# Kernel tuning notes

Measured on AMD Instinct MI355X. Metric: run time of the kernel, lower is better.

Reference implementation:

```python
import jax, jax.numpy as jnp
import numpy as np
from jax import lax

NUM_DISP = 64
BLOCK = 21
EPS = 1e-12  # F.normalize default eps


def _box_sum(v):
    # v: (N, H, W) -> BLOCK x BLOCK zero-padded box sum (same shape), separable.
    p = BLOCK // 2
    v = v[:, None]  # (N,1,H,W)
    kv = jnp.ones((1, 1, BLOCK, 1), v.dtype)
    kh = jnp.ones((1, 1, 1, BLOCK), v.dtype)
    v = lax.conv_general_dilated(v, kv, (1, 1), ((p, p), (0, 0)))
    v = lax.conv_general_dilated(v, kh, (1, 1), ((0, 0), (p, p)))
    return v[:, 0]


def _l2norm_c(img):
    n = jnp.sqrt(jnp.sum(img * img, axis=1, keepdims=True))
    return img / jnp.maximum(n, EPS)


def _disparity(left, right):
    # left, right: (B, 3, H, W)
    left = _l2norm_c(left)
    right = _l2norm_c(right)
    B, C, H, W = left.shape
    d = jnp.arange(NUM_DISP)
    xs = jnp.arange(W)
    idx = xs[None, :] - d[:, None]              # (D, W): source column in right image
    valid = (idx >= 0)
    r_shift = right[:, :, :, jnp.clip(idx, 0)]  # (B, C, H, D, W)
    r_shift = jnp.where(valid[None, None, None], r_shift, 0.0)
    # per-pixel channel-summed absolute difference -> (B, D, H, W)
    diff = jnp.sum(jnp.abs(left[:, :, :, None, :] - r_shift), axis=1)  # (B, H, D, W)
    diff = jnp.transpose(diff, (0, 2, 1, 3))    # (B, D, H, W)
    cost = _box_sum(diff.reshape(B * NUM_DISP, H, W)).reshape(B, NUM_DISP, H, W)
    cost = cost / (C * BLOCK * BLOCK)           # mean SAD over block elements
    return jnp.argmin(cost, axis=1).astype(left.dtype)  # (B, H, W)


def setup_inputs() -> dict:
    key = jax.random.key(0)
    k1, k2 = jax.random.split(key)
    x = jax.random.normal(k1, (2, 6, 320, 512), dtype=jnp.float32)
    gt = jax.random.normal(k2, (2, 6, 320, 512), dtype=jnp.float32)
    return {"x": x, "gt": gt}


def reference(x, gt):
    disp_gt = _disparity(gt[:, :3], gt[:, 3:])
    disp_pred = _disparity(x[:, :3], x[:, 3:])
    return jnp.mean(jnp.abs(disp_pred - disp_gt))
```

## Files before the change

### kernel.cpp

```cpp
#include <hip/hip_runtime.h>
#include <math.h>

constexpr int B = 2, H = 320, W = 512, D = 64;
constexpr int HW = H * W;
constexpr int R = 10;
constexpr int SEG = 80;
constexpr int NSEG = H / SEG;
constexpr int RS = 548;
constexpr float EPS = 1e-12f;

__global__ void k_norm(const float* __restrict__ x, const float* __restrict__ gt,
                       float4* __restrict__ nrm4) {
    int idx = blockIdx.x * blockDim.x + threadIdx.x;
    if (idx >= 2 * B * HW) return;
    int t = idx / (B * HW);
    int rem = idx - t * (B * HW);
    int b = rem / HW;
    int hw = rem - b * HW;
    const float* p = (t == 0 ? x : gt) + (size_t)b * 6 * HW + hw;
    float v0 = p[0],      v1 = p[HW],     v2 = p[2 * HW];
    float v3 = p[3 * HW], v4 = p[4 * HW], v5 = p[5 * HW];
    float n1 = fmaxf(sqrtf(v0 * v0 + v1 * v1 + v2 * v2), EPS);
    float n2 = fmaxf(sqrtf(v3 * v3 + v4 * v4 + v5 * v5), EPS);
    float4* q = nrm4 + (size_t)(t * B + b) * 2 * HW + hw;
    q[0]  = make_float4(v0 / n1, v1 / n1, v2 / n1, 0.f);
    q[HW] = make_float4(v3 / n2, v4 / n2, v5 / n2, 0.f);
}

__global__ __launch_bounds__(512, 2) void k_cost(const float4* __restrict__ nrm4,
                                                 float* __restrict__ cost, int t) {
    int blk = blockIdx.x;
    int combo = blk & 7;
    int d = blk >> 3;
    int b = combo >> 2;
    int seg = combo & 3;
    int w = threadIdx.x;
    const float4* L4 = nrm4 + (size_t)(t * B + b) * 2 * HW;
    const float4* R4 = L4 + HW;
    const bool val = (w >= d);
    const int wr = val ? (w - d) : 0;
    const int h0 = seg * SEG;

    __shared__ float ring[21][W];
    __shared__ float vsb[2][8][RS];

    {
        int j = w >> 6, k = w & 63;
        if (k < 10)      { vsb[0][j][k] = 0.f;       vsb[1][j][k] = 0.f; }
        else if (k < 20) { vsb[0][j][512 + k] = 0.f; vsb[1][j][512 + k] = 0.f; }
    }

    auto diff = [&](int h) -> float {
        float4 l = L4[(size_t)h * W + w];
        if (val) {
            float4 r = R4[(size_t)h * W + wr];
            return fabsf(l.x - r.x) + fabsf(l.y - r.y) + fabsf(l.z - r.z);
        }
        return fabsf(l.x) + fabsf(l.y) + fabsf(l.z);
    };

    float vs = 0.f;
    for (int k = 0; k < 20; ++k) {
        int h = h0 - R + k;
        float dv0 = (h >= 0) ? diff(h) : 0.f;
        ring[k][w] = dv0;
        vs += dv0;
    }
    ring[20][w] = 0.f;

    float* cp = cost + ((size_t)(b * D + d) * H) * W;
    const int cc = threadIdx.x >> 3;
    const int jj = threadIdx.x & 7;

    int slot0 = 20;
    for (int ss = 0; ss < SEG / 8; ++ss) {
        int sl[8];
        float dold[8], dv[8];
#pragma unroll
        for (int j = 0; j < 8; ++j) { int s2 = slot0 + j; if (s2 >= 21) s2 -= 21; sl[j] = s2; }
#pragma unroll
        for (int j = 0; j < 8; ++j) dold[j] = ring[sl[j]][w];
#pragma unroll
        for (int j = 0; j < 8; ++j) {
            int hn = h0 + ss * 8 + j + R;
            dv[j] = (hn < H) ? diff(hn) : 0.f;
        }
#pragma unroll
        for (int j = 0; j < 8; ++j) ring[sl[j]][w] = dv[j];
        float* vrow = &vsb[ss & 1][0][0];
#pragma unroll
        for (int j = 0; j < 8; ++j) { vs += dv[j] - dold[j]; vrow[j * RS + 10 + w] = vs; }
        __syncthreads();
        const float* vp = &vsb[ss & 1][jj][8 * cc];
        float wnd[28];
#pragma unroll
        for (int q = 0; q < 7; ++q) {
            float4 v4 = *(const float4*)(vp + 4 * q);
            wnd[4 * q] = v4.x; wnd[4 * q + 1] = v4.y;
            wnd[4 * q + 2] = v4.z; wnd[4 * q + 3] = v4.w;
        }
        float o = 0.f;
#pragma unroll
        for (int k = 0; k < 21; ++k) o += wnd[k];
        float out[8];
        out[0] = o;
#pragma unroll
        for (int k = 1; k < 8; ++k) { o += wnd[20 + k] - wnd[k - 1]; out[k] = o; }
        float* op = cp + (size_t)(h0 + ss * 8 + jj) * W + 8 * cc;
        *(float4*)(op)     = make_float4(out[0], out[1], out[2], out[3]);
        *(float4*)(op + 4) = make_float4(out[4], out[5], out[6], out[7]);
        slot0 += 8; if (slot0 >= 21) slot0 -= 21;
    }
}

__global__ void k_argmin0(const float* __restrict__ cost, float* __restrict__ disp) {
    int idx = blockIdx.x * 256 + threadIdx.x;
    if (idx >= B * HW) return;
    int b = idx / HW, hw = idx - b * HW;
    const float* cp = cost + (size_t)b * D * HW + hw;
    float best = cp[0]; int bd = 0;
#pragma unroll 16
    for (int d = 1; d < D; ++d) {
        float v = cp[(size_t)d * HW];
        if (v < best) { best = v; bd = d; }
    }
    disp[idx] = (float)bd;
}

__global__ void k_argmin1(const float* __restrict__ cost, const float* __restrict__ disp0,
                          float* __restrict__ part) {
    int idx = blockIdx.x * 256 + threadIdx.x;
    float s = 0.f;
    if (idx < B * HW) {
        int b = idx / HW, hw = idx - b * HW;
        const float* cp = cost + (size_t)b * D * HW + hw;
        float best = cp[0]; int bd = 0;
#pragma unroll 16
        for (int d = 1; d < D; ++d) {
            float v = cp[(size_t)d * HW];
            if (v < best) { best = v; bd = d; }
        }
        s = fabsf((float)bd - disp0[idx]);
    }
    __shared__ float sm[256];
    sm[threadIdx.x] = s;
    __syncthreads();
    for (int off = 128; off; off >>= 1) {
        if (threadIdx.x < off) sm[threadIdx.x] += sm[threadIdx.x + off];
        __syncthreads();
    }
    if (!threadIdx.x) part[blockIdx.x] = sm[0];
}

__global__ void k_red2(const float* __restrict__ part, float* __restrict__ out,
                       int nb, float inv) {
    __shared__ float sm[256];
    int tid = threadIdx.x;
    float s = 0.f;
    for (int i = tid; i < nb; i += 256) s += part[i];
    sm[tid] = s;
    __syncthreads();
    for (int off = 128; off; off >>= 1) {
        if (tid < off) sm[tid] += sm[tid + off];
        __syncthreads();
    }
    if (!tid) out[0] = sm[0] * inv;
}

extern "C" void kernel_launch(void* const* d_in, const int* in_sizes, int n_in,
                              void* d_out, int out_size, void* d_ws, size_t ws_size,
                              hipStream_t stream) {
    const float* x  = (const float*)d_in[0];
    const float* gt = (const float*)d_in[1];

    float4* nrm4 = (float4*)d_ws;
    float* cost  = (float*)(nrm4 + (size_t)2 * B * 2 * HW);
    float* disp  = cost + (size_t)B * D * HW;
    float* part  = disp + (size_t)2 * B * HW;

    constexpr int NPIX_BLKS = (B * HW + 255) / 256;

    k_norm<<<(2 * B * HW + 255) / 256, 256, 0, stream>>>(x, gt, nrm4);

    k_cost<<<B * NSEG * D, 512, 0, stream>>>(nrm4, cost, 0);
    k_argmin0<<<NPIX_BLKS, 256, 0, stream>>>(cost, disp);
    k_cost<<<B * NSEG * D, 512, 0, stream>>>(nrm4, cost, 1);
    k_argmin1<<<NPIX_BLKS, 256, 0, stream>>>(cost, disp, part);

    k_red2<<<1, 256, 0, stream>>>(part, (float*)d_out, NPIX_BLKS, 1.f / (float)(B * HW));
}
```

Measured before the change: 205.1 us.

## Fuse first argmin into second cost kernel and move ring buffer to registers

The argmin over the first image pair's cost volume now runs inside the second cost kernel. Each block reads a slice of the previous cost volume interleaved with its own work, which removes a separate argmin launch and lets those reads overlap with compute. This needs a second cost buffer in the workspace, with a fallback path when the workspace is too small. The 21-row shared-memory ring buffer becomes a fully unrolled 24-entry register ring, and the diff is made branch-free. This frees LDS but raises register pressure under launch bounds of 512 threads and 2 blocks.

Measured after the change: 198.4 us. 3.3% less time.

```diff
diff --git a/kernel.cpp b/kernel.cpp
--- a/kernel.cpp
+++ b/kernel.cpp
@@ -27,23 +27,24 @@
     q[HW] = make_float4(v3 / n2, v4 / n2, v5 / n2, 0.f);
 }
 
+template<bool FUSE>
 __global__ __launch_bounds__(512, 2) void k_cost(const float4* __restrict__ nrm4,
-                                                 float* __restrict__ cost, int t) {
-    int blk = blockIdx.x;
-    int combo = blk & 7;
-    int d = blk >> 3;
-    int b = combo >> 2;
-    int seg = combo & 3;
-    int w = threadIdx.x;
+                                                 float* __restrict__ cost,
+                                                 const float* __restrict__ cprev,
+                                                 float* __restrict__ dprev, int t) {
+    const int blk = blockIdx.x;
+    const int combo = blk & 7;
+    const int d = blk >> 3;
+    const int b = combo >> 2;
+    const int seg = combo & 3;
+    const int w = threadIdx.x;
     const float4* L4 = nrm4 + (size_t)(t * B + b) * 2 * HW;
     const float4* R4 = L4 + HW;
     const bool val = (w >= d);
     const int wr = val ? (w - d) : 0;
     const int h0 = seg * SEG;
 
-    __shared__ float ring[21][W];
     __shared__ float vsb[2][8][RS];
-
     {
         int j = w >> 6, k = w & 63;
         if (k < 10)      { vsb[0][j][k] = 0.f;       vsb[1][j][k] = 0.f; }
@@ -52,44 +53,71 @@
 
     auto diff = [&](int h) -> float {
         float4 l = L4[(size_t)h * W + w];
-        if (val) {
-            float4 r = R4[(size_t)h * W + wr];
-            return fabsf(l.x - r.x) + fabsf(l.y - r.y) + fabsf(l.z - r.z);
-        }
-        return fabsf(l.x) + fabsf(l.y) + fabsf(l.z);
+        float4 r = R4[(size_t)h * W + wr];
+        float a = fabsf(l.x - r.x) + fabsf(l.y - r.y) + fabsf(l.z - r.z);
+        float s = fabsf(l.x) + fabsf(l.y) + fabsf(l.z);
+        return val ? a : s;
     };
 
+    float ring[24];
     float vs = 0.f;
+#pragma unroll
     for (int k = 0; k < 20; ++k) {
         int h = h0 - R + k;
-        float dv0 = (h >= 0) ? diff(h) : 0.f;
-        ring[k][w] = dv0;
-        vs += dv0;
-    }
-    ring[20][w] = 0.f;
-
-    float* cp = cost + ((size_t)(b * D + d) * H) * W;
+        float dv = (h >= 0) ? diff(h) : 0.f;
+        ring[k] = dv;
+        vs += dv;
+    }
+    ring[20] = 0.f; ring[21] = 0.f; ring[22] = 0.f; ring[23] = 0.f;
+
+    const float* cp0 = nullptr; const float* cp1 = nullptr;
+    int px0 = 0, px1 = 0;
+    float best0 = 3.4e38f, best1 = 3.4e38f;
+    int bd0 = 0, bd1 = 0;
+    if (FUSE) {
+        px0 = blk * 640 + w;
+        int b0 = (px0 >= HW) ? 1 : 0;
+        cp0 = cprev + (size_t)b0 * D * HW + (px0 - b0 * HW);
+        if (w < 128) {
+            px1 = blk * 640 + 512 + w;
+            int b1 = (px1 >= HW) ? 1 : 0;
+            cp1 = cprev + (size_t)b1 * D * HW + (px1 - b1 * HW);
+        }
+    }
+
     const int cc = threadIdx.x >> 3;
     const int jj = threadIdx.x & 7;
-
-    int slot0 = 20;
-    for (int ss = 0; ss < SEG / 8; ++ss) {
-        int sl[8];
-        float dold[8], dv[8];
-#pragma unroll
-        for (int j = 0; j < 8; ++j) { int s2 = slot0 + j; if (s2 >= 21) s2 -= 21; sl[j] = s2; }
-#pragma unroll
-        for (int j = 0; j < 8; ++j) dold[j] = ring[sl[j]][w];
+    float* cp = cost + ((size_t)(b * D + d) * H) * W;
+
+    int dc = 0;
+#pragma unroll
+    for (int ss = 0; ss < 10; ++ss) {
+        const int nd = (ss < 4) ? 7 : 6;
+        float dvv[8];
 #pragma unroll
         for (int j = 0; j < 8; ++j) {
             int hn = h0 + ss * 8 + j + R;
-            dv[j] = (hn < H) ? diff(hn) : 0.f;
-        }
-#pragma unroll
-        for (int j = 0; j < 8; ++j) ring[sl[j]][w] = dv[j];
+            dvv[j] = (hn < H) ? diff(hn) : 0.f;
+        }
+        float fv0[7], fv1[7];
+        if (FUSE) {
+#pragma unroll
+            for (int q = 0; q < 7; ++q)
+                if (q < nd) fv0[q] = cp0[(size_t)(dc + q) * HW];
+            if (w < 128) {
+#pragma unroll
+                for (int q = 0; q < 7; ++q)
+                    if (q < nd) fv1[q] = cp1[(size_t)(dc + q) * HW];
+            }
+        }
         float* vrow = &vsb[ss & 1][0][0];
 #pragma unroll
-        for (int j = 0; j < 8; ++j) { vs += dv[j] - dold[j]; vrow[j * RS + 10 + w] = vs; }
+        for (int j = 0; j < 8; ++j) {
+            int i = ss * 8 + j;
+            vs += dvv[j] - ring[(i + 23) % 24];
+            ring[(i + 20) % 24] = dvv[j];
+            vrow[j * RS + 10 + w] = vs;
+        }
         __syncthreads();
         const float* vp = &vsb[ss & 1][jj][8 * cc];
         float wnd[28];
@@ -109,17 +137,31 @@
         float* op = cp + (size_t)(h0 + ss * 8 + jj) * W + 8 * cc;
         *(float4*)(op)     = make_float4(out[0], out[1], out[2], out[3]);
         *(float4*)(op + 4) = make_float4(out[4], out[5], out[6], out[7]);
-        slot0 += 8; if (slot0 >= 21) slot0 -= 21;
+        if (FUSE) {
+#pragma unroll
+            for (int q = 0; q < 7; ++q)
+                if (q < nd && fv0[q] < best0) { best0 = fv0[q]; bd0 = dc + q; }
+            if (w < 128) {
+#pragma unroll
+                for (int q = 0; q < 7; ++q)
+                    if (q < nd && fv1[q] < best1) { best1 = fv1[q]; bd1 = dc + q; }
+            }
+        }
+        dc += nd;
+    }
+    if (FUSE) {
+        dprev[px0] = (float)bd0;
+        if (w < 128) dprev[px1] = (float)bd1;
     }
 }
 
 __global__ void k_argmin0(const float* __restrict__ cost, float* __restrict__ disp) {
     int idx = blockIdx.x * 256 + threadIdx.x;
     if (idx >= B * HW) return;
-    int b = idx / HW, hw = idx - b * HW;
-    const float* cp = cost + (size_t)b * D * HW + hw;
+    int b = (idx >= HW) ? 1 : 0;
+    const float* cp = cost + (size_t)b * D * HW + (idx - b * HW);
     float best = cp[0]; int bd = 0;
-#pragma unroll 16
+#pragma unroll 8
     for (int d = 1; d < D; ++d) {
         float v = cp[(size_t)d * HW];
         if (v < best) { best = v; bd = d; }
@@ -127,15 +169,15 @@
     disp[idx] = (float)bd;
 }
 
-__global__ void k_argmin1(const float* __restrict__ cost, const float* __restrict__ disp0,
-                          float* __restrict__ part) {
+__global__ void k_final(const float* __restrict__ cost1, const float* __restrict__ disp0,
+                        float* __restrict__ part) {
     int idx = blockIdx.x * 256 + threadIdx.x;
     float s = 0.f;
     if (idx < B * HW) {
-        int b = idx / HW, hw = idx - b * HW;
-        const float* cp = cost + (size_t)b * D * HW + hw;
+        int b = (idx >= HW) ? 1 : 0;
+        const float* cp = cost1 + (size_t)b * D * HW + (idx - b * HW);
         float best = cp[0]; int bd = 0;
-#pragma unroll 16
+#pragma unroll 8
         for (int d = 1; d < D; ++d) {
             float v = cp[(size_t)d * HW];
             if (v < best) { best = v; bd = d; }
@@ -173,19 +215,33 @@
     const float* x  = (const float*)d_in[0];
     const float* gt = (const float*)d_in[1];
 
+    constexpr size_t NRM_F4 = (size_t)2 * B * 2 * HW;
+    constexpr size_t COST_F = (size_t)B * D * HW;
+    constexpr int NPIX_BLKS = (B * HW + 255) / 256;
+    constexpr int NRM_BLKS  = (2 * B * HW + 255) / 256;
+
     float4* nrm4 = (float4*)d_ws;
-    float* cost  = (float*)(nrm4 + (size_t)2 * B * 2 * HW);
-    float* disp  = cost + (size_t)B * D * HW;
-    float* part  = disp + (size_t)2 * B * HW;
-
-    constexpr int NPIX_BLKS = (B * HW + 255) / 256;
-
-    k_norm<<<(2 * B * HW + 255) / 256, 256, 0, stream>>>(x, gt, nrm4);
-
-    k_cost<<<B * NSEG * D, 512, 0, stream>>>(nrm4, cost, 0);
-    k_argmin0<<<NPIX_BLKS, 256, 0, stream>>>(cost, disp);
-    k_cost<<<B * NSEG * D, 512, 0, stream>>>(nrm4, cost, 1);
-    k_argmin1<<<NPIX_BLKS, 256, 0, stream>>>(cost, disp, part);
-
-    k_red2<<<1, 256, 0, stream>>>(part, (float*)d_out, NPIX_BLKS, 1.f / (float)(B * HW));
-}
+    float* cost0 = (float*)(nrm4 + NRM_F4);
+
+    size_t need_primary = NRM_F4 * 16 + 2 * COST_F * 4 + (size_t)(B * HW + 4096) * 4;
+
+    k_norm<<<NRM_BLKS, 256, 0, stream>>>(x, gt, nrm4);
+
+    if (ws_size >= need_primary) {
+        float* cost1 = cost0 + COST_F;
+        float* disp0 = cost1 + COST_F;
+        float* part  = disp0 + (size_t)B * HW;
+        k_cost<false><<<B * NSEG * D, 512, 0, stream>>>(nrm4, cost0, nullptr, nullptr, 0);
+        k_cost<true><<<B * NSEG * D, 512, 0, stream>>>(nrm4, cost1, cost0, disp0, 1);
+        k_final<<<NPIX_BLKS, 256, 0, stream>>>(cost1, disp0, part);
+        k_red2<<<1, 256, 0, stream>>>(part, (float*)d_out, NPIX_BLKS, 1.f / (float)(B * HW));
+    } else {
+        float* disp0 = cost0 + COST_F;
+        float* part  = disp0 + (size_t)B * HW;
+        k_cost<false><<<B * NSEG * D, 512, 0, stream>>>(nrm4, cost0, nullptr, nullptr, 0);
+        k_argmin0<<<NPIX_BLKS, 256, 0, stream>>>(cost0, disp0);
+        k_cost<false><<<B * NSEG * D, 512, 0, stream>>>(nrm4, cost0, nullptr, nullptr, 1);
+        k_final<<<NPIX_BLKS, 256, 0, stream>>>(cost0, disp0, part);
+        k_red2<<<1, 256, 0, stream>>>(part, (float*)d_out, NPIX_BLKS, 1.f / (float)(B * HW));
+    }
+}
```
